# Performance work log

Measured on AMD Instinct MI355X. Metric: run time of the kernel, lower is better.

Reference implementation:

```python
import jax, jax.numpy as jnp
import numpy as np

WIN = 7            # skimage default win_size
K1 = 0.01
K2 = 0.03
DATA_RANGE = 1.0   # images are in [0, 1]
PAD = (WIN - 1) // 2


def _uniform_filter_valid(x):
    # x: [N, 1, H, W] -> valid 7x7 box filter (== skimage uniform_filter cropped by PAD)
    k = jnp.ones((1, 1, WIN, WIN), x.dtype) / (WIN * WIN)
    return jax.lax.conv_general_dilated(
        x, k, window_strides=(1, 1), padding='VALID',
        dimension_numbers=('NCHW', 'OIHW', 'NCHW'))


def _ssim_mean(a, b):
    # a, b: [B, C, H, W]; each [H, W] slice is one independent SSIM image
    B, C, H, W = a.shape
    x = a.reshape(B * C, 1, H, W)
    y = b.reshape(B * C, 1, H, W)

    ux = _uniform_filter_valid(x)
    uy = _uniform_filter_valid(y)
    uxx = _uniform_filter_valid(x * x)
    uyy = _uniform_filter_valid(y * y)
    uxy = _uniform_filter_valid(x * y)

    NP = WIN * WIN
    cov_norm = NP / (NP - 1.0)  # sample covariance correction (skimage default)
    vx = cov_norm * (uxx - ux * ux)
    vy = cov_norm * (uyy - uy * uy)
    vxy = cov_norm * (uxy - ux * uy)

    C1 = (K1 * DATA_RANGE) ** 2
    C2 = (K2 * DATA_RANGE) ** 2

    S = ((2.0 * ux * uy + C1) * (2.0 * vxy + C2)) / \
        ((ux * ux + uy * uy + C1) * (vx + vy + C2))

    # skimage crops PAD border then means; VALID conv already cropped it.
    # All images are the same size, so np.average(per-image means) == global mean.
    return jnp.mean(S)


def setup_inputs() -> dict:
    key = jax.random.key(0)
    k1, k2 = jax.random.split(key)
    pred = jax.random.uniform(k1, (32, 4, 384, 384), dtype=jnp.float32)
    actual = jax.random.uniform(k2, (32, 4, 384, 384), dtype=jnp.float32)
    return {"pred": pred, "actual": actual}


def reference(pred, actual):
    return _ssim_mean(pred, actual)
```

## Files before the change

### kernel.cpp

```cpp
#include <hip/hip_runtime.h>

#define WIN 7
#define OUT_W 126
#define OUT_H 16
#define IN_W 132
#define IN_H 22
#define APITCH 532
#define H 384
#define W 384
#define OH 378
#define OW 378
#define NIMG 128
#define TX 3
#define TY 24
#define NBLK (TX * TY * NIMG)

__device__ __forceinline__ float wave_reduce(float v) {
#pragma unroll
    for (int off = 32; off > 0; off >>= 1) v += __shfl_down(v, off, 64);
    return v;
}

__global__ __launch_bounds__(256, 4) void ssim_main(const float* __restrict__ pred,
                                                    const float* __restrict__ act,
                                                    float* __restrict__ partials) {
    __shared__ __align__(16) float A[OUT_H * APITCH + 4];
    __shared__ float red[4];

    const int t = threadIdx.x;
    const int x0 = blockIdx.x * OUT_W;
    const int y0 = blockIdx.y * OUT_H;
    const size_t base = (size_t)blockIdx.z * H * W;

    if (t < IN_W) {
        const int col = x0 + t;
        const float* xc = pred + base + col;
        const float* yc = act + base + col;
        float xv[IN_H], yv[IN_H];
#pragma unroll
        for (int i = 0; i < IN_H; ++i) {
            const int row = y0 + i;
            const bool ok = row < H;
            xv[i] = ok ? xc[(size_t)row * W] : 0.f;
            yv[i] = ok ? yc[(size_t)row * W] : 0.f;
        }
        float sx = 0.f, sy = 0.f, sq = 0.f, sxy = 0.f;
#pragma unroll
        for (int k = 0; k < WIN; ++k) {
            sx += xv[k];
            sy += yv[k];
            sq = fmaf(xv[k], xv[k], fmaf(yv[k], yv[k], sq));
            sxy = fmaf(xv[k], yv[k], sxy);
        }
        float* ap = &A[t * 4];
        *(float4*)ap = make_float4(sx, sy, sq, sxy);
#pragma unroll
        for (int r = 1; r < OUT_H; ++r) {
            const float xn = xv[r + 6], yn = yv[r + 6];
            const float xo = xv[r - 1], yo = yv[r - 1];
            sx += xn - xo;
            sy += yn - yo;
            sq = fmaf(xn, xn, fmaf(yn, yn, fmaf(-xo, xo, fmaf(-yo, yo, sq))));
            sxy = fmaf(xn, yn, fmaf(-xo, yo, sxy));
            *(float4*)(ap + r * APITCH) = make_float4(sx, sy, sq, sxy);
        }
    }
    __syncthreads();

    const int r = t & 15;
    const int g = t >> 4;
    const int c0 = g * 8;

    const float C1B = 0.2401f;
    const float C2B = 2.1168f;

    const float4* qp = (const float4*)&A[r * APITCH + c0 * 4];
    float4 q[14];
#pragma unroll
    for (int k = 0; k < 14; ++k) q[k] = qp[k];

    float acc = 0.f;
    if (y0 + r < OH) {
        float Sx = 0.f, Sy = 0.f, Sq = 0.f, Sxy = 0.f;
#pragma unroll
        for (int k = 0; k < WIN - 1; ++k) {
            Sx += q[k].x; Sy += q[k].y; Sq += q[k].z; Sxy += q[k].w;
        }
#pragma unroll
        for (int j = 0; j < 8; ++j) {
            Sx += q[j + 6].x; Sy += q[j + 6].y; Sq += q[j + 6].z; Sxy += q[j + 6].w;

            const float p = Sx * Sy;
            const float qq = fmaf(Sx, Sx, Sy * Sy);
            const float n1 = fmaf(2.f, p, C1B);
            const float n2 = fmaf(98.f, Sxy, fmaf(-2.f, p, C2B));
            const float d1 = qq + C1B;
            const float d2 = fmaf(49.f, Sq, C2B - qq);
            const float s = (n1 * n2) * __builtin_amdgcn_rcpf(d1 * d2);
            acc = (c0 + j < OUT_W) ? acc + s : acc;

            Sx -= q[j].x; Sy -= q[j].y; Sq -= q[j].z; Sxy -= q[j].w;
        }
    }

    const float wsum = wave_reduce(acc);
    if ((t & 63) == 0) red[t >> 6] = wsum;
    __syncthreads();
    if (t == 0) {
        partials[blockIdx.x + TX * (blockIdx.y + TY * blockIdx.z)] =
            red[0] + red[1] + red[2] + red[3];
    }
}

__global__ __launch_bounds__(1024) void ssim_finalize(const float* __restrict__ partials,
                                                      float* __restrict__ out) {
    __shared__ double red[1024];
    const int t = threadIdx.x;
    double s = 0.0;
    for (int i = t; i < NBLK; i += 1024) s += (double)partials[i];
    red[t] = s;
    __syncthreads();
#pragma unroll
    for (int off = 512; off > 0; off >>= 1) {
        if (t < off) red[t] += red[t + off];
        __syncthreads();
    }
    if (t == 0) out[0] = (float)(red[0] / ((double)NIMG * OH * OW));
}

extern "C" void kernel_launch(void* const* d_in, const int* in_sizes, int n_in,
                              void* d_out, int out_size, void* d_ws, size_t ws_size,
                              hipStream_t stream) {
    const float* pred = (const float*)d_in[0];
    const float* act  = (const float*)d_in[1];
    float* partials = (float*)d_ws;
    dim3 grid(TX, TY, NIMG);
    ssim_main<<<grid, 256, 0, stream>>>(pred, act, partials);
    ssim_finalize<<<1, 1024, 0, stream>>>(partials, (float*)d_out);
}
```

Before: 174.4 us.

## Store vertical box sums as packed bf16 in LDS with mean-centered inputs

Inputs are shifted by 0.5 before the vertical box sums so the sums stay small and bf16 truncation error is reduced. The four partial sums are then packed into two 32-bit words per column (bf16 pairs) in two planar LDS arrays, which halves shared memory per block so occupancy can rise (launch bounds raised to 6). The horizontal pass unpacks them and undoes the centering for the mean terms. This trades accuracy, since bf16 truncation of the variance and covariance sums may change the result, for less LDS traffic and more resident blocks.

```diff
diff --git a/kernel.cpp b/kernel.cpp
--- a/kernel.cpp
+++ b/kernel.cpp
@@ -1,11 +1,13 @@
 #include <hip/hip_runtime.h>
+#include <stdint.h>
 
 #define WIN 7
 #define OUT_W 126
 #define OUT_H 16
 #define IN_W 132
 #define IN_H 22
-#define APITCH 532
+#define PITCH 140
+#define AELEM (OUT_H * PITCH)
 #define H 384
 #define W 384
 #define OH 378
@@ -21,10 +23,21 @@
     return v;
 }
 
-__global__ __launch_bounds__(256, 4) void ssim_main(const float* __restrict__ pred,
+__device__ __forceinline__ uint32_t pack2(float lo, float hi) {
+    return (__builtin_bit_cast(uint32_t, hi) & 0xFFFF0000u) |
+           (__builtin_bit_cast(uint32_t, lo) >> 16);
+}
+__device__ __forceinline__ float unpk_lo(uint32_t w) {
+    return __builtin_bit_cast(float, w << 16);
+}
+__device__ __forceinline__ float unpk_hi(uint32_t w) {
+    return __builtin_bit_cast(float, w & 0xFFFF0000u);
+}
+
+__global__ __launch_bounds__(256, 6) void ssim_main(const float* __restrict__ pred,
                                                     const float* __restrict__ act,
                                                     float* __restrict__ partials) {
-    __shared__ __align__(16) float A[OUT_H * APITCH + 4];
+    __shared__ __align__(16) uint32_t P[2 * AELEM];
     __shared__ float red[4];
 
     const int t = threadIdx.x;
@@ -41,8 +54,8 @@
         for (int i = 0; i < IN_H; ++i) {
             const int row = y0 + i;
             const bool ok = row < H;
-            xv[i] = ok ? xc[(size_t)row * W] : 0.f;
-            yv[i] = ok ? yc[(size_t)row * W] : 0.f;
+            xv[i] = ok ? (xc[(size_t)row * W] - 0.5f) : 0.f;
+            yv[i] = ok ? (yc[(size_t)row * W] - 0.5f) : 0.f;
         }
         float sx = 0.f, sy = 0.f, sq = 0.f, sxy = 0.f;
 #pragma unroll
@@ -52,8 +65,8 @@
             sq = fmaf(xv[k], xv[k], fmaf(yv[k], yv[k], sq));
             sxy = fmaf(xv[k], yv[k], sxy);
         }
-        float* ap = &A[t * 4];
-        *(float4*)ap = make_float4(sx, sy, sq, sxy);
+        P[t] = pack2(sx, sy);
+        P[AELEM + t] = pack2(sq, sxy);
 #pragma unroll
         for (int r = 1; r < OUT_H; ++r) {
             const float xn = xv[r + 6], yn = yv[r + 6];
@@ -62,7 +75,9 @@
             sy += yn - yo;
             sq = fmaf(xn, xn, fmaf(yn, yn, fmaf(-xo, xo, fmaf(-yo, yo, sq))));
             sxy = fmaf(xn, yn, fmaf(-xo, yo, sxy));
-            *(float4*)(ap + r * APITCH) = make_float4(sx, sy, sq, sxy);
+            const int a = r * PITCH + t;
+            P[a] = pack2(sx, sy);
+            P[AELEM + a] = pack2(sq, sxy);
         }
     }
     __syncthreads();
@@ -74,32 +89,48 @@
     const float C1B = 0.2401f;
     const float C2B = 2.1168f;
 
-    const float4* qp = (const float4*)&A[r * APITCH + c0 * 4];
-    float4 q[14];
-#pragma unroll
-    for (int k = 0; k < 14; ++k) q[k] = qp[k];
-
     float acc = 0.f;
     if (y0 + r < OH) {
-        float Sx = 0.f, Sy = 0.f, Sq = 0.f, Sxy = 0.f;
+        float S[4][8];
 #pragma unroll
-        for (int k = 0; k < WIN - 1; ++k) {
-            Sx += q[k].x; Sy += q[k].y; Sq += q[k].z; Sxy += q[k].w;
+        for (int a = 0; a < 2; ++a) {
+            const uint32_t* bp = &P[a * AELEM + r * PITCH + c0];
+            uint32_t w[16];
+#pragma unroll
+            for (int k = 0; k < 4; ++k) {
+                const uint4 q = ((const uint4*)bp)[k];
+                w[4 * k + 0] = q.x; w[4 * k + 1] = q.y;
+                w[4 * k + 2] = q.z; w[4 * k + 3] = q.w;
+            }
+            float vlo[16], vhi[16];
+#pragma unroll
+            for (int k = 0; k < 16; ++k) { vlo[k] = unpk_lo(w[k]); vhi[k] = unpk_hi(w[k]); }
+            float slo = ((vlo[0] + vlo[1]) + (vlo[2] + vlo[3])) + ((vlo[4] + vlo[5]) + vlo[6]);
+            float shi = ((vhi[0] + vhi[1]) + (vhi[2] + vhi[3])) + ((vhi[4] + vhi[5]) + vhi[6]);
+            S[2 * a][0] = slo;
+            S[2 * a + 1][0] = shi;
+#pragma unroll
+            for (int j = 1; j < 8; ++j) {
+                slo += vlo[j + 6] - vlo[j - 1];
+                shi += vhi[j + 6] - vhi[j - 1];
+                S[2 * a][j] = slo;
+                S[2 * a + 1][j] = shi;
+            }
         }
+        const int nmax = OUT_W - c0;
 #pragma unroll
         for (int j = 0; j < 8; ++j) {
-            Sx += q[j + 6].x; Sy += q[j + 6].y; Sq += q[j + 6].z; Sxy += q[j + 6].w;
-
-            const float p = Sx * Sy;
-            const float qq = fmaf(Sx, Sx, Sy * Sy);
-            const float n1 = fmaf(2.f, p, C1B);
-            const float n2 = fmaf(98.f, Sxy, fmaf(-2.f, p, C2B));
-            const float d1 = qq + C1B;
-            const float d2 = fmaf(49.f, Sq, C2B - qq);
+            const float Sxc = S[0][j], Syc = S[1][j];
+            const float Sqc = S[2][j], Sxyc = S[3][j];
+            const float pc = Sxc * Syc;
+            const float qc = fmaf(Sxc, Sxc, Syc * Syc);
+            const float n2 = fmaf(98.f, Sxyc, fmaf(-2.f, pc, C2B));
+            const float d2 = fmaf(49.f, Sqc, C2B - qc);
+            const float Sx = Sxc + 24.5f, Sy = Syc + 24.5f;
+            const float n1 = fmaf(2.f, Sx * Sy, C1B);
+            const float d1 = fmaf(Sx, Sx, fmaf(Sy, Sy, C1B));
             const float s = (n1 * n2) * __builtin_amdgcn_rcpf(d1 * d2);
-            acc = (c0 + j < OUT_W) ? acc + s : acc;
-
-            Sx -= q[j].x; Sy -= q[j].y; Sq -= q[j].z; Sxy -= q[j].w;
+            acc = (j < nmax) ? acc + s : acc;
         }
     }
 
```

Measured after the change: 221.6 us. 27.1% more time.
